# Optimization experiments

Measured on AMD Instinct MI355X. Metric: run time of the kernel, lower is better.

## Reference

```python
import jax, jax.numpy as jnp
import numpy as np

B, T, H, DK, DV = 4, 2048, 1024, 1024, 1024


def setup_inputs() -> dict:
    key = jax.random.key(0)
    ks = jax.random.split(key, 9)
    s = lambda fan_in: 1.0 / np.sqrt(fan_in)
    return {
        "y_all": jax.random.normal(ks[0], (B, T, H), dtype=jnp.float32),
        "Wq": jax.random.uniform(ks[1], (H, DK), jnp.float32, -s(H), s(H)),
        "bq": jax.random.uniform(ks[2], (DK,), jnp.float32, -s(H), s(H)),
        "Wk": jax.random.uniform(ks[3], (H, DK), jnp.float32, -s(H), s(H)),
        "bk": jax.random.uniform(ks[4], (DK,), jnp.float32, -s(H), s(H)),
        "Wv": jax.random.uniform(ks[5], (H, DV), jnp.float32, -s(H), s(H)),
        "bv": jax.random.uniform(ks[6], (DV,), jnp.float32, -s(H), s(H)),
        "Wo": jax.random.uniform(ks[7], (DV, H), jnp.float32, -s(DV), s(DV)),
        "bo": jax.random.uniform(ks[8], (H,), jnp.float32, -s(DV), s(DV)),
    }


def reference(y_all, Wq, bq, Wk, bk, Wv, bv, Wo, bo):
    # Fused causal attention equivalent to the per-timestep Python loop.
    dk = Wq.shape[1]
    q = (y_all @ Wq + bq) / jnp.sqrt(jnp.asarray(dk, y_all.dtype))  # [B,T,DK]
    k = y_all @ Wk + bk                                             # [B,T,DK]
    v = y_all @ Wv + bv                                             # [B,T,DV]
    scores = jnp.einsum("bqd,bkd->bqk", q, k)                       # [B,T,T]
    t = y_all.shape[1]
    causal = jnp.tril(jnp.ones((t, t), dtype=bool))                 # [T,T]
    scores = jnp.where(causal[None], scores, jnp.asarray(-jnp.inf, scores.dtype))
    w = jax.nn.softmax(scores, axis=-1)                             # [B,T,T]
    ctx = jnp.einsum("bqk,bkd->bqd", w, v)                          # [B,T,DV]
    return ctx @ Wo + bo                                            # [B,T,H]
```

## Files before the change

### kernel.cpp

```cpp
#include <hip/hip_runtime.h>
#include <hip/hip_bf16.h>
#include <cstdint>

#define DEVI __device__ __forceinline__

typedef __attribute__((ext_vector_type(8))) short bf16x8;
typedef __attribute__((ext_vector_type(4))) short bf16x4;
typedef __attribute__((ext_vector_type(4))) float f32x4;

DEVI short f2bf(float f) {
  unsigned u = __float_as_uint(f);
  u += 0x7fff + ((u >> 16) & 1);
  return (short)(u >> 16);
}
DEVI float bf2f(short s) { return __uint_as_float(((unsigned)(unsigned short)s) << 16); }

DEVI void gl_lds16(const short* g, short* l) {
  __builtin_amdgcn_global_load_lds((const __attribute__((address_space(1))) unsigned*)g,
                                   (__attribute__((address_space(3))) unsigned*)l, 16, 0, 0);
}


__global__ __launch_bounds__(256, 4)
void gemm_ww(const short* __restrict__ WkBf, const short* __restrict__ WqBf,
             const short* __restrict__ WoT, const short* __restrict__ WvBf,
             float* __restrict__ partM, float* __restrict__ partW)
{
  const int orig = blockIdx.x;
  const int xcd = orig & 7, idx8 = orig >> 3;
  const int wg = xcd * 64 + idx8;
  const int job = wg >> 8, rem = wg & 255;
  const int z = rem >> 6, t = rem & 63;
  const int bi = t >> 3, bj = t & 7;

  const short* A = job ? WoT  : WkBf;
  const short* B = job ? WvBf : WqBf;
  float* Cf = (job ? partW : partM) + (long long)z * 1048576;

  __shared__ __align__(16) short lA[128 * 64];
  __shared__ __align__(16) short lB[128 * 64];

  const int tid = threadIdx.x, wave = tid >> 6, lane = tid & 63;
  const int wr = wave >> 1, wc = wave & 1;
  const int brow = bi * 128, bcol = bj * 128;
  const int fr = lane & 15, h = lane >> 4;

  const int ck0 = ((h ^ (fr & 7))) * 8;
  const int swc = ((tid & 7) ^ ((tid >> 3) & 7)) * 8;
  const short* pA = A + (long long)(brow + (tid >> 3)) * 1024 + swc;
  const short* pB = B + (long long)(bcol + (tid >> 3)) * 1024 + swc;

  f32x4 acc[4][4] = {};
  const long long ko0 = (long long)z * 256;

  for (int t2 = 0; t2 < 4; ++t2) {
    const long long ko = ko0 + t2 * 64;
#pragma unroll
    for (int j = 0; j < 4; ++j)
      gl_lds16(pA + (long long)(j * 32) * 1024 + ko, &lA[j * 2048 + tid * 8]);
#pragma unroll
    for (int j = 0; j < 4; ++j)
      gl_lds16(pB + (long long)(j * 32) * 1024 + ko, &lB[j * 2048 + tid * 8]);
    __syncthreads();

    bf16x8 af[4], bg[4];
#pragma unroll
    for (int m = 0; m < 4; ++m)
      af[m] = *(const bf16x8*)&lA[(wr * 64 + m * 16 + fr) * 64 + ck0];
#pragma unroll
    for (int n = 0; n < 4; ++n)
      bg[n] = *(const bf16x8*)&lB[(wc * 64 + n * 16 + fr) * 64 + ck0];
#pragma unroll
    for (int m = 0; m < 4; ++m)
#pragma unroll
      for (int n = 0; n < 4; ++n)
        acc[m][n] = __builtin_amdgcn_mfma_f32_16x16x32_bf16(af[m], bg[n], acc[m][n], 0, 0, 0);
#pragma unroll
    for (int m = 0; m < 4; ++m)
      af[m] = *(const bf16x8*)&lA[((wr * 64 + m * 16 + fr) * 64 + ck0) ^ 32];
#pragma unroll
    for (int n = 0; n < 4; ++n)
      bg[n] = *(const bf16x8*)&lB[((wc * 64 + n * 16 + fr) * 64 + ck0) ^ 32];
#pragma unroll
    for (int m = 0; m < 4; ++m)
#pragma unroll
      for (int n = 0; n < 4; ++n)
        acc[m][n] = __builtin_amdgcn_mfma_f32_16x16x32_bf16(af[m], bg[n], acc[m][n], 0, 0, 0);
    __syncthreads();
  }

  const int lrow = h * 4;
#pragma unroll
  for (int m = 0; m < 4; ++m) {
    const int row = brow + wr * 64 + m * 16 + lrow;
#pragma unroll
    for (int j = 0; j < 4; ++j)
#pragma unroll
      for (int n = 0; n < 4; ++n)
        Cf[(long long)(row + j) * 1024 + bcol + wc * 64 + n * 16 + fr] = acc[m][n][j];
  }
}

__global__ __launch_bounds__(256)
void combine_ww(const float* __restrict__ partM, const float* __restrict__ partW,
                short* __restrict__ MTb, short* __restrict__ WvoT)
{
  const int wg = blockIdx.x;
  const float* p = (wg < 1024) ? partM : partW;
  short* out = (wg < 1024) ? MTb : WvoT;
  const long long i = (long long)(wg & 1023) * 256 + threadIdx.x;
  const float4 a = ((const float4*)p)[i];
  const float4 b = ((const float4*)(p + 1048576))[i];
  const float4 c = ((const float4*)(p + 2097152))[i];
  const float4 d = ((const float4*)(p + 3145728))[i];
  bf16x4 o;
  o[0] = f2bf(a.x + b.x + c.x + d.x);
  o[1] = f2bf(a.y + b.y + c.y + d.y);
  o[2] = f2bf(a.z + b.z + c.z + d.z);
  o[3] = f2bf(a.w + b.w + c.w + d.w);
  ((bf16x4*)out)[i] = o;
}

__global__ __launch_bounds__(256, 6)
void gemm_g2(const short* __restrict__ ybf, const short* __restrict__ MTb,
             short* __restrict__ G, const float* __restrict__ wvec)
{
  const int orig = blockIdx.x;
  const int xcd = orig & 7, idx8 = orig >> 3;
  const int wg = xcd * 128 + idx8;
  const int bi = wg >> 4, bj = wg & 15;

  __shared__ __align__(16) short lA[128 * 64];
  __shared__ __align__(16) short lB[64 * 64];

  const int tid = threadIdx.x, wave = tid >> 6, lane = tid & 63;
  const int wr = wave >> 1, wc = wave & 1;
  const int brow = bi * 128, bcol = bj * 64;
  const int fr = lane & 15, h = lane >> 4;

  const int ck0 = ((h ^ (fr & 7))) * 8;
  const int swc = ((tid & 7) ^ ((tid >> 3) & 7)) * 8;
  const short* pA = ybf + (long long)(brow + (tid >> 3)) * 1024 + swc;
  const short* pB = MTb + (long long)(bcol + (tid >> 3)) * 1024 + swc;

  f32x4 acc[4][2] = {};

  for (int t = 0; t < 16; ++t) {
    const long long ko = (long long)t * 64;
#pragma unroll
    for (int j = 0; j < 4; ++j)
      gl_lds16(pA + (long long)(j * 32) * 1024 + ko, &lA[j * 2048 + tid * 8]);
#pragma unroll
    for (int j = 0; j < 2; ++j)
      gl_lds16(pB + (long long)(j * 32) * 1024 + ko, &lB[j * 2048 + tid * 8]);
    __syncthreads();

    bf16x8 af[4], bg[2];
#pragma unroll
    for (int m = 0; m < 4; ++m)
      af[m] = *(const bf16x8*)&lA[(wr * 64 + m * 16 + fr) * 64 + ck0];
#pragma unroll
    for (int n = 0; n < 2; ++n)
      bg[n] = *(const bf16x8*)&lB[(wc * 32 + n * 16 + fr) * 64 + ck0];
#pragma unroll
    for (int m = 0; m < 4; ++m)
#pragma unroll
      for (int n = 0; n < 2; ++n)
        acc[m][n] = __builtin_amdgcn_mfma_f32_16x16x32_bf16(af[m], bg[n], acc[m][n], 0, 0, 0);
#pragma unroll
    for (int m = 0; m < 4; ++m)
      af[m] = *(const bf16x8*)&lA[((wr * 64 + m * 16 + fr) * 64 + ck0) ^ 32];
#pragma unroll
    for (int n = 0; n < 2; ++n)
      bg[n] = *(const bf16x8*)&lB[((wc * 32 + n * 16 + fr) * 64 + ck0) ^ 32];
#pragma unroll
    for (int m = 0; m < 4; ++m)
#pragma unroll
      for (int n = 0; n < 2; ++n)
        acc[m][n] = __builtin_amdgcn_mfma_f32_16x16x32_bf16(af[m], bg[n], acc[m][n], 0, 0, 0);
    __syncthreads();
  }

  const int lrow = h * 4;
  int colg[2]; float bvv[2];
#pragma unroll
  for (int n = 0; n < 2; ++n) {
    colg[n] = bcol + wc * 32 + n * 16 + fr;
    bvv[n] = wvec[colg[n]];
  }
#pragma unroll
  for (int m = 0; m < 4; ++m) {
    const int row = brow + wr * 64 + m * 16 + lrow;
#pragma unroll
    for (int j = 0; j < 4; ++j)
#pragma unroll
      for (int n = 0; n < 2; ++n)
        G[(long long)(row + j) * 1024 + colg[n]] =
            f2bf((acc[m][n][j] + bvv[n]) * (1.f / 32.f));
  }
}

__global__ __launch_bounds__(256, 6)
void gemm_sz2(const short* __restrict__ G, const short* __restrict__ ybf,
              const short* __restrict__ WvoT, short* __restrict__ scores,
              short* __restrict__ zT)
{
  const int orig = blockIdx.x;
  const int xcd = orig & 7, idx8 = orig >> 3;
  const int wg = xcd * 264 + idx8;

  const short *A, *B; short* C; int ldc, bi, bj;
  if (wg < 1088) {
    const int z = wg / 272, t = wg - z * 272;
    const int k = (t >= 20) + (t >= 72) + (t >= 156);
    const int u = t - (16 * k * k + 4 * k);
    int r, col;
    if (u < 32 * k) {
      const int cb = u >> 5, w = u & 31;
      r = w >> 3; col = cb * 8 + (w & 7);
    } else {
      const int u2 = u - 32 * k;
      r = (u2 >= 2) + (u2 >= 6) + (u2 >= 12);
      const int cum = (r == 0) ? 0 : (r == 1) ? 2 : (r == 2) ? 6 : 12;
      col = 8 * k + (u2 - cum);
    }
    bi = 4 * k + r; bj = col;
    A = G + (long long)z * 2048 * 1024;
    B = ybf + (long long)z * 2048 * 1024;
    C = scores + (long long)z * 2048 * 2048;
    ldc = 2048;
  } else {
    const int lwg = wg - 1088;
    bi = lwg >> 7; bj = lwg & 127;
    A = WvoT; B = ybf; C = zT; ldc = 8192;
  }

  __shared__ __align__(16) short lA[128 * 64];
  __shared__ __align__(16) short lB[64 * 64];

  const int tid = threadIdx.x, wave = tid >> 6, lane = tid & 63;
  const int wr = wave >> 1, wc = wave & 1;
  const int brow = bi * 128, bcol = bj * 64;
  const int fr = lane & 15, h = lane >> 4;

  const int ck0 = ((h ^ (fr & 7))) * 8;
  const int swc = ((tid & 7) ^ ((tid >> 3) & 7)) * 8;
  const short* pA = A + (long long)(brow + (tid >> 3)) * 1024 + swc;
  const short* pB = B + (long long)(bcol + (tid >> 3)) * 1024 + swc;

  f32x4 acc[4][2] = {};

  for (int t = 0; t < 16; ++t) {
    const long long ko = (long long)t * 64;
#pragma unroll
    for (int j = 0; j < 4; ++j)
      gl_lds16(pA + (long long)(j * 32) * 1024 + ko, &lA[j * 2048 + tid * 8]);
#pragma unroll
    for (int j = 0; j < 2; ++j)
      gl_lds16(pB + (long long)(j * 32) * 1024 + ko, &lB[j * 2048 + tid * 8]);
    __syncthreads();

    bf16x8 af[4], bg[2];
#pragma unroll
    for (int m = 0; m < 4; ++m)
      af[m] = *(const bf16x8*)&lA[(wr * 64 + m * 16 + fr) * 64 + ck0];
#pragma unroll
    for (int n = 0; n < 2; ++n)
      bg[n] = *(const bf16x8*)&lB[(wc * 32 + n * 16 + fr) * 64 + ck0];
#pragma unroll
    for (int m = 0; m < 4; ++m)
#pragma unroll
      for (int n = 0; n < 2; ++n)
        acc[m][n] = __builtin_amdgcn_mfma_f32_16x16x32_bf16(af[m], bg[n], acc[m][n], 0, 0, 0);
#pragma unroll
    for (int m = 0; m < 4; ++m)
      af[m] = *(const bf16x8*)&lA[((wr * 64 + m * 16 + fr) * 64 + ck0) ^ 32];
#pragma unroll
    for (int n = 0; n < 2; ++n)
      bg[n] = *(const bf16x8*)&lB[((wc * 32 + n * 16 + fr) * 64 + ck0) ^ 32];
#pragma unroll
    for (int m = 0; m < 4; ++m)
#pragma unroll
      for (int n = 0; n < 2; ++n)
        acc[m][n] = __builtin_amdgcn_mfma_f32_16x16x32_bf16(af[m], bg[n], acc[m][n], 0, 0, 0);
    __syncthreads();
  }

  const int lrow = h * 4;
  int colg[2];
#pragma unroll
  for (int n = 0; n < 2; ++n) colg[n] = bcol + wc * 32 + n * 16 + fr;
#pragma unroll
  for (int m = 0; m < 4; ++m) {
    const int row = brow + wr * 64 + m * 16 + lrow;
#pragma unroll
    for (int j = 0; j < 4; ++j)
#pragma unroll
      for (int n = 0; n < 2; ++n)
        C[(long long)(row + j) * ldc + colg[n]] = f2bf(acc[m][n][j]);
  }
}

__global__ __launch_bounds__(256, 6)
void gemm_pv(const short* __restrict__ scores, const short* __restrict__ zT,
             float* __restrict__ out, const float* __restrict__ bo,
             const float* __restrict__ bvWo)
{
  const int orig = blockIdx.x;
  const int xcd = orig & 7, idx8 = orig >> 3;
  const int z = xcd >> 1;
  const int bi = ((idx8 >> 4) << 1) | (xcd & 1);
  const int bj = idx8 & 15;

  const short* A = scores + (long long)z * 2048 * 2048;
  const int nt = bi + 1;

  __shared__ __align__(16) short lA[64 * 64];
  __shared__ __align__(16) short lB[64 * 64];

  const int tid = threadIdx.x, wave = tid >> 6, lane = tid & 63;
  const int wm = wave >> 1, wn = wave & 1;
  const int brow = bi * 64, bcol = bj * 64;
  const int fr = lane & 15, h = lane >> 4;

  const int ck0 = ((h ^ (fr & 7))) * 8;
  const int swc = ((tid & 7) ^ ((tid >> 3) & 7)) * 8;
  const short* pA = A + (long long)(brow + (tid >> 3)) * 2048 + swc;
  const short* pB = zT + (long long)(bcol + (tid >> 3)) * 8192 + z * 2048 + swc;

  f32x4 acc[2][2] = {};

  for (int t = 0; t < nt; ++t) {
    const long long ko = (long long)t * 64;
#pragma unroll
    for (int j = 0; j < 2; ++j)
      gl_lds16(pA + (long long)(j * 32) * 2048 + ko, &lA[j * 2048 + tid * 8]);
#pragma unroll
    for (int j = 0; j < 2; ++j)
      gl_lds16(pB + (long long)(j * 32) * 8192 + ko, &lB[j * 2048 + tid * 8]);
    __syncthreads();

    bf16x8 af[2], bg[2];
#pragma unroll
    for (int m = 0; m < 2; ++m)
      af[m] = *(const bf16x8*)&lA[(wm * 32 + m * 16 + fr) * 64 + ck0];
#pragma unroll
    for (int n = 0; n < 2; ++n)
      bg[n] = *(const bf16x8*)&lB[(wn * 32 + n * 16 + fr) * 64 + ck0];
#pragma unroll
    for (int m = 0; m < 2; ++m)
#pragma unroll
      for (int n = 0; n < 2; ++n)
        acc[m][n] = __builtin_amdgcn_mfma_f32_16x16x32_bf16(af[m], bg[n], acc[m][n], 0, 0, 0);
#pragma unroll
    for (int m = 0; m < 2; ++m)
      af[m] = *(const bf16x8*)&lA[((wm * 32 + m * 16 + fr) * 64 + ck0) ^ 32];
#pragma unroll
    for (int n = 0; n < 2; ++n)
      bg[n] = *(const bf16x8*)&lB[((wn * 32 + n * 16 + fr) * 64 + ck0) ^ 32];
#pragma unroll
    for (int m = 0; m < 2; ++m)
#pragma unroll
      for (int n = 0; n < 2; ++n)
        acc[m][n] = __builtin_amdgcn_mfma_f32_16x16x32_bf16(af[m], bg[n], acc[m][n], 0, 0, 0);
    __syncthreads();
  }

  const int lrow = h * 4;
  int colg[2]; float bvv[2];
#pragma unroll
  for (int n = 0; n < 2; ++n) {
    colg[n] = bcol + wn * 32 + n * 16 + fr;
    bvv[n] = bo[colg[n]] + bvWo[colg[n]];
  }
#pragma unroll
  for (int m = 0; m < 2; ++m) {
    const int row = brow + wm * 32 + m * 16 + lrow;
#pragma unroll
    for (int j = 0; j < 4; ++j)
#pragma unroll
      for (int n = 0; n < 2; ++n)
        out[(long long)(z * 2048 + row + j) * 1024 + colg[n]] = acc[m][n][j] + bvv[n];
  }
}

__global__ __launch_bounds__(256)
void softmax_causal_bf16_k(short* __restrict__ sc)
{
  const int T = 2048;
  const long long row = blockIdx.x;
  const int t = (int)(row & (T - 1));
  short* ps = sc + row * (long long)T;
  const int tid = threadIdx.x, wave = tid >> 6, lane = tid & 63;
  const int c0 = tid * 8;
  const int wlim = ((t >> 6) + 1) << 6;

  bf16x8 v = {};
  if (c0 <= t) v = *(const bf16x8*)&ps[c0];
  float x[8];
#pragma unroll
  for (int j = 0; j < 8; ++j) x[j] = bf2f(v[j]);

  float mx = -3.0e38f;
#pragma unroll
  for (int j = 0; j < 8; ++j) if (c0 + j <= t) mx = fmaxf(mx, x[j]);
#pragma unroll
  for (int o = 32; o; o >>= 1) mx = fmaxf(mx, __shfl_xor(mx, o, 64));
  __shared__ float red[8];
  if (lane == 0) red[wave] = mx;
  __syncthreads();
  const float M = fmaxf(fmaxf(red[0], red[1]), fmaxf(red[2], red[3]));

  float e[8], s = 0.f;
#pragma unroll
  for (int j = 0; j < 8; ++j) { e[j] = (c0 + j <= t) ? __expf(x[j] - M) : 0.f; s += e[j]; }
#pragma unroll
  for (int o = 32; o; o >>= 1) s += __shfl_xor(s, o, 64);
  if (lane == 0) red[4 + wave] = s;
  __syncthreads();
  const float inv = 1.f / (red[4] + red[5] + red[6] + red[7]);

  if (c0 < wlim) {
    bf16x8 ov;
#pragma unroll
    for (int j = 0; j < 8; ++j) ov[j] = f2bf(e[j] * inv);
    *(bf16x8*)&ps[c0] = ov;
  }
}

__global__ __launch_bounds__(256)
void cvt_all(const float* __restrict__ y, const float* __restrict__ Wq,
             const float* __restrict__ Wk, const float* __restrict__ Wo,
             const float* __restrict__ Wv, const float* __restrict__ bq,
             const float* __restrict__ bv,
             short* __restrict__ ybf, short* __restrict__ WqBf,
             short* __restrict__ WkBf, short* __restrict__ WoT,
             short* __restrict__ WvBf, float* __restrict__ wvec,
             float* __restrict__ bvWo)
{
  const int wg = blockIdx.x, tid = threadIdx.x;
  __shared__ float tile[32][33];
  __shared__ float red[4];

  if (wg < 4096) {
    const long long i = (long long)wg * 256 + tid;
    const float4 v0 = ((const float4*)y)[i * 2];
    const float4 v1 = ((const float4*)y)[i * 2 + 1];
    bf16x8 o;
    o[0] = f2bf(v0.x); o[1] = f2bf(v0.y); o[2] = f2bf(v0.z); o[3] = f2bf(v0.w);
    o[4] = f2bf(v1.x); o[5] = f2bf(v1.y); o[6] = f2bf(v1.z); o[7] = f2bf(v1.w);
    ((bf16x8*)ybf)[i] = o;
  } else if (wg < 8192) {
    const int lwg = wg - 4096;
    const int bx = lwg & 31, by = (lwg >> 5) & 31, bz = lwg >> 10;
    const int tx = tid & 31, ty = tid >> 5;
    const int r0 = by * 32, c0 = bx * 32;
    if (bz != 2) {
      const float* in = (bz == 0) ? Wq : (bz == 1 ? Wk : Wv);
      short* out      = (bz == 0) ? WqBf : (bz == 1 ? WkBf : WvBf);
#pragma unroll
      for (int i = 0; i < 4; ++i)
        out[(long long)(r0 + ty + 8 * i) * 1024 + c0 + tx] =
            f2bf(in[(long long)(r0 + ty + 8 * i) * 1024 + c0 + tx]);
    } else {
#pragma unroll
      for (int i = 0; i < 4; ++i)
        tile[ty + 8 * i][tx] = Wo[(long long)(r0 + ty + 8 * i) * 1024 + c0 + tx];
      __syncthreads();
#pragma unroll
      for (int i = 0; i < 4; ++i)
        WoT[(long long)(c0 + ty + 8 * i) * 1024 + r0 + tx] = f2bf(tile[tx][ty + 8 * i]);
    }
  } else if (wg < 9216) {
    const int row = wg - 8192;
    const float4 a = ((const float4*)(Wk + (long long)row * 1024))[tid];
    const float4 b = ((const float4*)bq)[tid];
    float s = a.x * b.x + a.y * b.y + a.z * b.z + a.w * b.w;
#pragma unroll
    for (int o = 32; o; o >>= 1) s += __shfl_xor(s, o, 64);
    if ((tid & 63) == 0) red[tid >> 6] = s;
    __syncthreads();
    if (tid == 0) wvec[row] = red[0] + red[1] + red[2] + red[3];
  } else {
    const int r0 = (wg - 9216) * 16;
    const int c4 = tid;
    float4 acc = make_float4(0.f, 0.f, 0.f, 0.f);
    for (int r = 0; r < 16; ++r) {
      const float s = bv[r0 + r];
      const float4 w = ((const float4*)(Wo + (long long)(r0 + r) * 1024))[c4];
      acc.x += s * w.x; acc.y += s * w.y; acc.z += s * w.z; acc.w += s * w.w;
    }
    atomicAdd(&bvWo[c4 * 4 + 0], acc.x);
    atomicAdd(&bvWo[c4 * 4 + 1], acc.y);
    atomicAdd(&bvWo[c4 * 4 + 2], acc.z);
    atomicAdd(&bvWo[c4 * 4 + 3], acc.w);
  }
}

extern "C" void kernel_launch(void* const* d_in, const int* in_sizes, int n_in,
                              void* d_out, int out_size, void* d_ws, size_t ws_size,
                              hipStream_t stream)
{
  (void)in_sizes; (void)n_in; (void)out_size; (void)ws_size;
  const float* y  = (const float*)d_in[0];
  const float* Wq = (const float*)d_in[1];
  const float* bq = (const float*)d_in[2];
  const float* Wk = (const float*)d_in[3];
  const float* bk = (const float*)d_in[4];
  const float* Wv = (const float*)d_in[5];
  const float* bv = (const float*)d_in[6];
  const float* Wo = (const float*)d_in[7];
  const float* bo = (const float*)d_in[8];
  float* out = (float*)d_out;
  (void)bk;

  const int T = 2048;
  const long long MT = 8192;
  const long long MM = 1048576;

  short* ws    = (short*)d_ws;
  short* ybf   = ws;
  short* WqBf  = ybf + MT * 1024;
  short* WkBf  = WqBf + MM;
  short* WoT   = WkBf + MM;
  short* WvBf  = WoT + MM;
  short* MTb   = WvBf + MM;
  short* WvoT  = MTb + MM;
  short* G     = WvoT + MM;
  short* zT    = G + MT * 1024;
  short* scores = zT + MT * 1024;
  float* bvWo  = (float*)(scores + 4ll * T * T);
  float* wvec  = bvWo + 1024;
  float* partM = wvec + 1024;
  float* partW = partM + 4ll * MM;

  hipMemsetAsync(bvWo, 0, 1024 * sizeof(float), stream);

  cvt_all<<<9280, 256, 0, stream>>>(y, Wq, Wk, Wo, Wv, bq, bv,
                                    ybf, WqBf, WkBf, WoT, WvBf, wvec, bvWo);

  gemm_ww<<<512, 256, 0, stream>>>(WkBf, WqBf, WoT, WvBf, partM, partW);
  combine_ww<<<2048, 256, 0, stream>>>(partM, partW, MTb, WvoT);

  gemm_g2<<<1024, 256, 0, stream>>>(ybf, MTb, G, wvec);

  gemm_sz2<<<2112, 256, 0, stream>>>(G, ybf, WvoT, scores, zT);

  softmax_causal_bf16_k<<<(int)MT, 256, 0, stream>>>(scores);

  gemm_pv<<<2048, 256, 0, stream>>>(scores, zT, out, bo, bvWo);
}
```

Baseline: 161.4 us.

## Drop split-K for weight-product GEMM and enlarge PV row tile to 128

The weight-product GEMM switches from 128x128 tiles with 4-way split-K plus a separate fp32 combine kernel to 64x64 tiles over the full K, writing bf16 directly. This removes the partial-sum traffic and one launch. The PV GEMM moves to 128-row tiles with 1024 blocks, which halves the number of B-operand reloads but uses coarser causal granularity and fewer blocks. The softmax zero-fill limit is widened to 128-column multiples to match the new PV tiles, and the block-to-row mapping is alternated for load balance.

```diff
diff --git a/kernel.cpp b/kernel.cpp
--- a/kernel.cpp
+++ b/kernel.cpp
@@ -21,28 +21,27 @@
 }
 
 
-__global__ __launch_bounds__(256, 4)
-void gemm_ww(const short* __restrict__ WkBf, const short* __restrict__ WqBf,
-             const short* __restrict__ WoT, const short* __restrict__ WvBf,
-             float* __restrict__ partM, float* __restrict__ partW)
+__global__ __launch_bounds__(256, 6)
+void gemm_ww64(const short* __restrict__ WkBf, const short* __restrict__ WqBf,
+               const short* __restrict__ WoT, const short* __restrict__ WvBf,
+               short* __restrict__ MTb, short* __restrict__ WvoT)
 {
   const int orig = blockIdx.x;
   const int xcd = orig & 7, idx8 = orig >> 3;
   const int wg = xcd * 64 + idx8;
   const int job = wg >> 8, rem = wg & 255;
-  const int z = rem >> 6, t = rem & 63;
-  const int bi = t >> 3, bj = t & 7;
+  const int bi = rem >> 4, bj = rem & 15;
 
   const short* A = job ? WoT  : WkBf;
   const short* B = job ? WvBf : WqBf;
-  float* Cf = (job ? partW : partM) + (long long)z * 1048576;
-
-  __shared__ __align__(16) short lA[128 * 64];
-  __shared__ __align__(16) short lB[128 * 64];
+  short* C = job ? WvoT : MTb;
+
+  __shared__ __align__(16) short lA[64 * 64];
+  __shared__ __align__(16) short lB[64 * 64];
 
   const int tid = threadIdx.x, wave = tid >> 6, lane = tid & 63;
-  const int wr = wave >> 1, wc = wave & 1;
-  const int brow = bi * 128, bcol = bj * 128;
+  const int wm = wave >> 1, wn = wave & 1;
+  const int brow = bi * 64, bcol = bj * 64;
   const int fr = lane & 15, h = lane >> 4;
 
   const int ck0 = ((h ^ (fr & 7))) * 8;
@@ -50,75 +49,54 @@
   const short* pA = A + (long long)(brow + (tid >> 3)) * 1024 + swc;
   const short* pB = B + (long long)(bcol + (tid >> 3)) * 1024 + swc;
 
-  f32x4 acc[4][4] = {};
-  const long long ko0 = (long long)z * 256;
-
-  for (int t2 = 0; t2 < 4; ++t2) {
-    const long long ko = ko0 + t2 * 64;
-#pragma unroll
-    for (int j = 0; j < 4; ++j)
+  f32x4 acc[2][2] = {};
+
+  for (int t = 0; t < 16; ++t) {
+    const long long ko = (long long)t * 64;
+#pragma unroll
+    for (int j = 0; j < 2; ++j)
       gl_lds16(pA + (long long)(j * 32) * 1024 + ko, &lA[j * 2048 + tid * 8]);
 #pragma unroll
-    for (int j = 0; j < 4; ++j)
+    for (int j = 0; j < 2; ++j)
       gl_lds16(pB + (long long)(j * 32) * 1024 + ko, &lB[j * 2048 + tid * 8]);
     __syncthreads();
 
-    bf16x8 af[4], bg[4];
-#pragma unroll
-    for (int m = 0; m < 4; ++m)
-      af[m] = *(const bf16x8*)&lA[(wr * 64 + m * 16 + fr) * 64 + ck0];
-#pragma unroll
-    for (int n = 0; n < 4; ++n)
-      bg[n] = *(const bf16x8*)&lB[(wc * 64 + n * 16 + fr) * 64 + ck0];
-#pragma unroll
-    for (int m = 0; m < 4; ++m)
-#pragma unroll
-      for (int n = 0; n < 4; ++n)
-        acc[m][n] = __builtin_amdgcn_mfma_f32_16x16x32_bf16(af[m], bg[n], acc[m][n], 0, 0, 0);
-#pragma unroll
-    for (int m = 0; m < 4; ++m)
-      af[m] = *(const bf16x8*)&lA[((wr * 64 + m * 16 + fr) * 64 + ck0) ^ 32];
-#pragma unroll
-    for (int n = 0; n < 4; ++n)
-      bg[n] = *(const bf16x8*)&lB[((wc * 64 + n * 16 + fr) * 64 + ck0) ^ 32];
-#pragma unroll
-    for (int m = 0; m < 4; ++m)
-#pragma unroll
-      for (int n = 0; n < 4; ++n)
+    bf16x8 af[2], bg[2];
+#pragma unroll
+    for (int m = 0; m < 2; ++m)
+      af[m] = *(const bf16x8*)&lA[(wm * 32 + m * 16 + fr) * 64 + ck0];
+#pragma unroll
+    for (int n = 0; n < 2; ++n)
+      bg[n] = *(const bf16x8*)&lB[(wn * 32 + n * 16 + fr) * 64 + ck0];
+#pragma unroll
+    for (int m = 0; m < 2; ++m)
+#pragma unroll
+      for (int n = 0; n < 2; ++n)
+        acc[m][n] = __builtin_amdgcn_mfma_f32_16x16x32_bf16(af[m], bg[n], acc[m][n], 0, 0, 0);
+#pragma unroll
+    for (int m = 0; m < 2; ++m)
+      af[m] = *(const bf16x8*)&lA[((wm * 32 + m * 16 + fr) * 64 + ck0) ^ 32];
+#pragma unroll
+    for (int n = 0; n < 2; ++n)
+      bg[n] = *(const bf16x8*)&lB[((wn * 32 + n * 16 + fr) * 64 + ck0) ^ 32];
+#pragma unroll
+    for (int m = 0; m < 2; ++m)
+#pragma unroll
+      for (int n = 0; n < 2; ++n)
         acc[m][n] = __builtin_amdgcn_mfma_f32_16x16x32_bf16(af[m], bg[n], acc[m][n], 0, 0, 0);
     __syncthreads();
   }
 
   const int lrow = h * 4;
 #pragma unroll
-  for (int m = 0; m < 4; ++m) {
-    const int row = brow + wr * 64 + m * 16 + lrow;
-#pragma unroll
-    for (int j = 0; j < 4; ++j)
-#pragma unroll
-      for (int n = 0; n < 4; ++n)
-        Cf[(long long)(row + j) * 1024 + bcol + wc * 64 + n * 16 + fr] = acc[m][n][j];
-  }
-}
-
-__global__ __launch_bounds__(256)
-void combine_ww(const float* __restrict__ partM, const float* __restrict__ partW,
-                short* __restrict__ MTb, short* __restrict__ WvoT)
-{
-  const int wg = blockIdx.x;
-  const float* p = (wg < 1024) ? partM : partW;
-  short* out = (wg < 1024) ? MTb : WvoT;
-  const long long i = (long long)(wg & 1023) * 256 + threadIdx.x;
-  const float4 a = ((const float4*)p)[i];
-  const float4 b = ((const float4*)(p + 1048576))[i];
-  const float4 c = ((const float4*)(p + 2097152))[i];
-  const float4 d = ((const float4*)(p + 3145728))[i];
-  bf16x4 o;
-  o[0] = f2bf(a.x + b.x + c.x + d.x);
-  o[1] = f2bf(a.y + b.y + c.y + d.y);
-  o[2] = f2bf(a.z + b.z + c.z + d.z);
-  o[3] = f2bf(a.w + b.w + c.w + d.w);
-  ((bf16x4*)out)[i] = o;
+  for (int m = 0; m < 2; ++m) {
+    const int row = brow + wm * 32 + m * 16 + lrow;
+#pragma unroll
+    for (int j = 0; j < 4; ++j)
+#pragma unroll
+      for (int n = 0; n < 2; ++n)
+        C[(long long)(row + j) * 1024 + bcol + wn * 32 + n * 16 + fr] = f2bf(acc[m][n][j]);
+  }
 }
 
 __global__ __launch_bounds__(256, 6)
@@ -309,18 +287,18 @@
   const int orig = blockIdx.x;
   const int xcd = orig & 7, idx8 = orig >> 3;
   const int z = xcd >> 1;
-  const int bi = ((idx8 >> 4) << 1) | (xcd & 1);
+  const int bi = ((idx8 >> 4) << 1) | ((xcd & 1) ^ (idx8 & 1));
   const int bj = idx8 & 15;
 
   const short* A = scores + (long long)z * 2048 * 2048;
-  const int nt = bi + 1;
-
-  __shared__ __align__(16) short lA[64 * 64];
+  const int nt = 2 * (bi + 1);
+
+  __shared__ __align__(16) short lA[128 * 64];
   __shared__ __align__(16) short lB[64 * 64];
 
   const int tid = threadIdx.x, wave = tid >> 6, lane = tid & 63;
-  const int wm = wave >> 1, wn = wave & 1;
-  const int brow = bi * 64, bcol = bj * 64;
+  const int wr = wave >> 1, wc = wave & 1;
+  const int brow = bi * 128, bcol = bj * 64;
   const int fr = lane & 15, h = lane >> 4;
 
   const int ck0 = ((h ^ (fr & 7))) * 8;
@@ -328,38 +306,38 @@
   const short* pA = A + (long long)(brow + (tid >> 3)) * 2048 + swc;
   const short* pB = zT + (long long)(bcol + (tid >> 3)) * 8192 + z * 2048 + swc;
 
-  f32x4 acc[2][2] = {};
+  f32x4 acc[4][2] = {};
 
   for (int t = 0; t < nt; ++t) {
     const long long ko = (long long)t * 64;
 #pragma unroll
-    for (int j = 0; j < 2; ++j)
+    for (int j = 0; j < 4; ++j)
       gl_lds16(pA + (long long)(j * 32) * 2048 + ko, &lA[j * 2048 + tid * 8]);
 #pragma unroll
     for (int j = 0; j < 2; ++j)
       gl_lds16(pB + (long long)(j * 32) * 8192 + ko, &lB[j * 2048 + tid * 8]);
     __syncthreads();
 
-    bf16x8 af[2], bg[2];
-#pragma unroll
-    for (int m = 0; m < 2; ++m)
-      af[m] = *(const bf16x8*)&lA[(wm * 32 + m * 16 + fr) * 64 + ck0];
-#pragma unroll
-    for (int n = 0; n < 2; ++n)
-      bg[n] = *(const bf16x8*)&lB[(wn * 32 + n * 16 + fr) * 64 + ck0];
-#pragma unroll
-    for (int m = 0; m < 2; ++m)
-#pragma unroll
-      for (int n = 0; n < 2; ++n)
-        acc[m][n] = __builtin_amdgcn_mfma_f32_16x16x32_bf16(af[m], bg[n], acc[m][n], 0, 0, 0);
-#pragma unroll
-    for (int m = 0; m < 2; ++m)
-      af[m] = *(const bf16x8*)&lA[((wm * 32 + m * 16 + fr) * 64 + ck0) ^ 32];
-#pragma unroll
-    for (int n = 0; n < 2; ++n)
-      bg[n] = *(const bf16x8*)&lB[((wn * 32 + n * 16 + fr) * 64 + ck0) ^ 32];
-#pragma unroll
-    for (int m = 0; m < 2; ++m)
+    bf16x8 af[4], bg[2];
+#pragma unroll
+    for (int m = 0; m < 4; ++m)
+      af[m] = *(const bf16x8*)&lA[(wr * 64 + m * 16 + fr) * 64 + ck0];
+#pragma unroll
+    for (int n = 0; n < 2; ++n)
+      bg[n] = *(const bf16x8*)&lB[(wc * 32 + n * 16 + fr) * 64 + ck0];
+#pragma unroll
+    for (int m = 0; m < 4; ++m)
+#pragma unroll
+      for (int n = 0; n < 2; ++n)
+        acc[m][n] = __builtin_amdgcn_mfma_f32_16x16x32_bf16(af[m], bg[n], acc[m][n], 0, 0, 0);
+#pragma unroll
+    for (int m = 0; m < 4; ++m)
+      af[m] = *(const bf16x8*)&lA[((wr * 64 + m * 16 + fr) * 64 + ck0) ^ 32];
+#pragma unroll
+    for (int n = 0; n < 2; ++n)
+      bg[n] = *(const bf16x8*)&lB[((wc * 32 + n * 16 + fr) * 64 + ck0) ^ 32];
+#pragma unroll
+    for (int m = 0; m < 4; ++m)
 #pragma unroll
       for (int n = 0; n < 2; ++n)
         acc[m][n] = __builtin_amdgcn_mfma_f32_16x16x32_bf16(af[m], bg[n], acc[m][n], 0, 0, 0);
@@ -370,12 +348,12 @@
   int colg[2]; float bvv[2];
 #pragma unroll
   for (int n = 0; n < 2; ++n) {
-    colg[n] = bcol + wn * 32 + n * 16 + fr;
+    colg[n] = bcol + wc * 32 + n * 16 + fr;
     bvv[n] = bo[colg[n]] + bvWo[colg[n]];
   }
 #pragma unroll
-  for (int m = 0; m < 2; ++m) {
-    const int row = brow + wm * 32 + m * 16 + lrow;
+  for (int m = 0; m < 4; ++m) {
+    const int row = brow + wr * 64 + m * 16 + lrow;
 #pragma unroll
     for (int j = 0; j < 4; ++j)
 #pragma unroll
@@ -393,7 +371,7 @@
   short* ps = sc + row * (long long)T;
   const int tid = threadIdx.x, wave = tid >> 6, lane = tid & 63;
   const int c0 = tid * 8;
-  const int wlim = ((t >> 6) + 1) << 6;
+  const int wlim = ((t >> 7) + 1) << 7;
 
   bf16x8 v = {};
   if (c0 <= t) v = *(const bf16x8*)&ps[c0];
@@ -531,16 +509,13 @@
   short* scores = zT + MT * 1024;
   float* bvWo  = (float*)(scores + 4ll * T * T);
   float* wvec  = bvWo + 1024;
-  float* partM = wvec + 1024;
-  float* partW = partM + 4ll * MM;
 
   hipMemsetAsync(bvWo, 0, 1024 * sizeof(float), stream);
 
   cvt_all<<<9280, 256, 0, stream>>>(y, Wq, Wk, Wo, Wv, bq, bv,
                                     ybf, WqBf, WkBf, WoT, WvBf, wvec, bvWo);
 
-  gemm_ww<<<512, 256, 0, stream>>>(WkBf, WqBf, WoT, WvBf, partM, partW);
-  combine_ww<<<2048, 256, 0, stream>>>(partM, partW, MTb, WvoT);
+  gemm_ww64<<<512, 256, 0, stream>>>(WkBf, WqBf, WoT, WvBf, MTb, WvoT);
 
   gemm_g2<<<1024, 256, 0, stream>>>(ybf, MTb, G, wvec);
 
@@ -548,5 +523,5 @@
 
   softmax_causal_bf16_k<<<(int)MT, 256, 0, stream>>>(scores);
 
-  gemm_pv<<<2048, 256, 0, stream>>>(scores, zT, out, bo, bvWo);
-}
+  gemm_pv<<<1024, 256, 0, stream>>>(scores, zT, out, bo, bvWo);
+}
```

Result: faster. 154.8 us (median of 2 runs) (-4.1%).
